# Kernel tuning notes

Hardware: AMD Instinct MI355X
Metric: run time of the kernel (lower is better)

## Reference

```python
import jax, jax.numpy as jnp
import numpy as np

N_NODES = 20000
N_EDGES = 1280000
IN_CH = 256
HID_CH = 256


def setup_inputs() -> dict:
    key = jax.random.key(0)
    ks = jax.random.split(key, 8)
    s = 1.0 / np.sqrt(IN_CH)
    sh = 1.0 / np.sqrt(HID_CH)
    return {
        "x": jax.random.normal(ks[0], (N_NODES, IN_CH), dtype=jnp.float32),
        "edge_index": jax.random.randint(ks[1], (2, N_EDGES), 0, N_NODES, dtype=jnp.int64),
        "W1_l": jax.random.normal(ks[2], (HID_CH, IN_CH), dtype=jnp.float32) * s,
        "b1": jnp.zeros((HID_CH,), dtype=jnp.float32),
        "W1_r": jax.random.normal(ks[3], (HID_CH, IN_CH), dtype=jnp.float32) * s,
        "W2_l": jax.random.normal(ks[4], (1, HID_CH), dtype=jnp.float32) * sh,
        "b2": jnp.zeros((1,), dtype=jnp.float32),
        "W2_r": jax.random.normal(ks[5], (1, HID_CH), dtype=jnp.float32) * sh,
        "fc_w": jax.random.normal(ks[6], (1, N_NODES), dtype=jnp.float32) * (1.0 / np.sqrt(N_NODES)),
        "fc_b": jnp.zeros((1,), dtype=jnp.float32),
    }


def _sage(x, src, dst, inv_deg, W_l, b, W_r):
    # mean-aggregate source features at destination nodes, then two linears
    agg = jax.ops.segment_sum(x[src], dst, num_segments=N_NODES)  # [N, C]
    mean = agg * inv_deg[:, None]
    return mean @ W_l.T + b + x @ W_r.T


def reference(x, edge_index, W1_l, b1, W1_r, W2_l, b2, W2_r, fc_w, fc_b):
    src, dst = edge_index[0], edge_index[1]
    deg = jax.ops.segment_sum(jnp.ones((dst.shape[0],), dtype=x.dtype), dst,
                              num_segments=N_NODES)
    inv_deg = 1.0 / jnp.maximum(deg, 1.0)  # isolated nodes -> 0 aggregate
    h = jax.nn.relu(_sage(x, src, dst, inv_deg, W1_l, b1, W1_r))   # [N, H]
    h = jax.nn.relu(_sage(h, src, dst, inv_deg, W2_l, b2, W2_r))   # [N, 1]
    h = h[:, 0]                                                     # squeeze dim 1
    return h @ fc_w[0] + fc_b                                       # [1]
```

## Files before the change

kernel.cpp:

```cpp
#include <hip/hip_runtime.h>

#define N_NODESC 20000
#define N_EDGESC 1280000
#define NB 256
#define EPB 5000

typedef short bf16x8 __attribute__((ext_vector_type(8)));
typedef float f32x4 __attribute__((ext_vector_type(4)));

constexpr size_t OFF_DEG      = 0;
constexpr size_t OFF_ROWSTART = 81920;
constexpr size_t OFF_INVDEG   = 163840;
constexpr size_t OFF_BSUM     = 245760;
constexpr size_t OFF_BOFF     = 246272;
constexpr size_t OFF_S1       = 246784;
constexpr size_t OFF_T1       = 326784;
constexpr size_t OFF_PART     = 406784;
constexpr size_t OFF_HIST     = 427264;
constexpr size_t OFF_CSR      = 10667264;
constexpr size_t OFF_XB       = 13227392;
constexpr size_t OFF_MEANB    = 23467392;
constexpr size_t OFF_W1LB     = 33707392;
constexpr size_t OFF_W1RB     = 33838464;

static __device__ __forceinline__ unsigned f2bf(float f) {
    unsigned u = __float_as_uint(f);
    return ((u + 0x7fffu + ((u >> 16) & 1u)) >> 16) & 0xffffu;
}
static __device__ __forceinline__ float bflo(unsigned w) {
    return __uint_as_float(w << 16);
}
static __device__ __forceinline__ float bfhi(unsigned w) {
    return __uint_as_float(w & 0xffff0000u);
}

__global__ void __launch_bounds__(256) k_cast(
        const float4* __restrict__ x, const float4* __restrict__ w1l,
        const float4* __restrict__ w1r, uint4* __restrict__ xb,
        uint4* __restrict__ w1lb, uint4* __restrict__ w1rb,
        float* __restrict__ s1, float* __restrict__ t1,
        int* __restrict__ bsum) {
    int g = blockIdx.x * 256 + threadIdx.x;
    if (g < N_NODESC) { s1[g] = 0.0f; t1[g] = 0.0f; }
    if (g < 128) bsum[g] = 0;
    const float4* src; uint4* dst; int off;
    if (g < 640000)      { src = x;   dst = xb;   off = g; }
    else if (g < 648192) { src = w1l; dst = w1lb; off = g - 640000; }
    else                 { src = w1r; dst = w1rb; off = g - 648192; }
    float4 a = src[off * 2], b = src[off * 2 + 1];
    uint4 o;
    o.x = f2bf(a.x) | (f2bf(a.y) << 16);
    o.y = f2bf(a.z) | (f2bf(a.w) << 16);
    o.z = f2bf(b.x) | (f2bf(b.y) << 16);
    o.w = f2bf(b.z) | (f2bf(b.w) << 16);
    dst[off] = o;
}

__global__ void __launch_bounds__(256) k_hist(const int* __restrict__ ei,
                                              unsigned short* __restrict__ hist) {
    __shared__ unsigned int lh[10000];
    int b = blockIdx.x, t = threadIdx.x;
    for (int w = t; w < 10000; w += 256) lh[w] = 0;
    __syncthreads();
    int base = b * EPB;
    for (int i = t; i < EPB; i += 256) {
        int d = ei[N_EDGESC + base + i];
        atomicAdd(&lh[d >> 1], (d & 1) ? 0x10000u : 1u);
    }
    __syncthreads();
    unsigned int* gh = (unsigned int*)(hist + (size_t)b * N_NODESC);
    for (int w = t; w < 10000; w += 256) gh[w] = lh[w];
}

__global__ void __launch_bounds__(256) k_prefix(unsigned short* __restrict__ hist,
                                                int* __restrict__ deg,
                                                int* __restrict__ bsum) {
    __shared__ int wtot[4][64];
    int t = threadIdx.x;
    int lb = t & 63, sub = t >> 6;
    int bin = blockIdx.x * 64 + lb;
    bool ok = bin < N_NODESC;
    int vals[64];
    int run = 0;
    if (ok) {
        #pragma unroll
        for (int i = 0; i < 64; i++) {
            vals[i] = hist[(size_t)(sub * 64 + i) * N_NODESC + bin];
            run += vals[i];
        }
    }
    wtot[sub][lb] = run;
    __syncthreads();
    int off = 0, total = 0;
    for (int w = 0; w < 4; w++) {
        int v = wtot[w][lb];
        if (w < sub) off += v;
        total += v;
    }
    if (sub == 0) {
        int tv = ok ? total : 0;
        if (ok) deg[bin] = total;
        #pragma unroll
        for (int o2 = 32; o2 > 0; o2 >>= 1) tv += __shfl_down(tv, o2);
        if (lb == 0) atomicAdd(&bsum[(blockIdx.x * 64) >> 8], tv);
    }
    if (ok) {
        int run2 = off;
        #pragma unroll
        for (int i = 0; i < 64; i++) {
            hist[(size_t)(sub * 64 + i) * N_NODESC + bin] = (unsigned short)run2;
            run2 += vals[i];
        }
    }
}

__global__ void k_scan2(const int* __restrict__ bsum, int* __restrict__ boff,
                        int* __restrict__ row_start) {
    __shared__ int sm[128];
    int t = threadIdx.x;
    int v = (t < 79) ? bsum[t] : 0;
    sm[t] = v;
    __syncthreads();
    for (int off = 1; off < 128; off <<= 1) {
        int add = (t >= off) ? sm[t - off] : 0;
        __syncthreads();
        sm[t] += add;
        __syncthreads();
    }
    if (t < 79) boff[t] = sm[t] - v;
    if (t == 0) row_start[N_NODESC] = sm[127];
}

__global__ void __launch_bounds__(256) k_scan3(
        const int* __restrict__ deg, const int* __restrict__ boff,
        int* __restrict__ row_start, float* __restrict__ inv_deg) {
    __shared__ int wsum[4];
    int i = blockIdx.x * 256 + threadIdx.x;
    int lane = threadIdx.x & 63, wid = threadIdx.x >> 6;
    int v = (i < N_NODESC) ? deg[i] : 0;
    int incl = v;
    #pragma unroll
    for (int off = 1; off < 64; off <<= 1) {
        int n = __shfl_up(incl, off);
        if (lane >= off) incl += n;
    }
    if (lane == 63) wsum[wid] = incl;
    __syncthreads();
    int wpre = 0;
    #pragma unroll
    for (int w = 0; w < 4; w++) wpre += (w < wid) ? wsum[w] : 0;
    if (i < N_NODESC) {
        row_start[i] = boff[blockIdx.x] + wpre + incl - v;
        inv_deg[i]   = 1.0f / (float)max(v, 1);
    }
}

__global__ void __launch_bounds__(256) k_fill2(const int* __restrict__ ei,
        const int* __restrict__ row_start, const unsigned short* __restrict__ hist,
        unsigned short* __restrict__ csr) {
    __shared__ unsigned int lh[10000];
    int b = blockIdx.x, t = threadIdx.x;
    for (int w = t; w < 10000; w += 256) lh[w] = 0;
    __syncthreads();
    int base = b * EPB;
    const unsigned short* hb = hist + (size_t)b * N_NODESC;
    for (int i = t; i < EPB; i += 256) {
        int e = base + i;
        int d = ei[N_EDGESC + e];
        int s = ei[e];
        unsigned int old = atomicAdd(&lh[d >> 1], (d & 1) ? 0x10000u : 1u);
        int rank = (d & 1) ? (int)(old >> 16) : (int)(old & 0xffffu);
        int pos = row_start[d] + (int)hb[d] + rank;
        csr[pos] = (unsigned short)s;
    }
}

__global__ void __launch_bounds__(256) k_agg(const char* __restrict__ xbc,
        const int* __restrict__ row_start, const unsigned short* __restrict__ csr,
        const float* __restrict__ inv_deg, uint4* __restrict__ meanb4) {
    int wid = threadIdx.x >> 6, lane = threadIdx.x & 63;
    int node = blockIdx.x * 4 + wid;
    int pass = blockIdx.y;
    int ol = lane & 7, oct = lane >> 3;
    unsigned lanebyte = ((unsigned)(pass << 3) + (unsigned)ol) << 4;
    int start = row_start[node], end = row_start[node + 1];
    float a0=0.f,a1=0.f,a2=0.f,a3=0.f,a4=0.f,a5=0.f,a6=0.f,a7=0.f;
    float c0=0.f,c1=0.f,c2=0.f,c3=0.f,c4=0.f,c5=0.f,c6=0.f,c7=0.f;
    int idx = (start < end) ? (int)csr[start + lane] : 0;
    for (int j = start; j < end; j += 64) {
        int cnt = min(64, end - j);
        int idxn = (j + 64 < end) ? (int)csr[j + 64 + lane] : 0;
        int fs = cnt >> 3;
        int k = 0;
        for (; k + 2 <= fs; k += 2) {
            int s0 = __shfl(idx, 8 * k + oct);
            int s1 = __shfl(idx, 8 * k + 8 + oct);
            uint4 v0 = *(const uint4*)(xbc + (((unsigned)s0 << 9) + lanebyte));
            uint4 v1 = *(const uint4*)(xbc + (((unsigned)s1 << 9) + lanebyte));
            a0 += bflo(v0.x); a1 += bfhi(v0.x); a2 += bflo(v0.y); a3 += bfhi(v0.y);
            a4 += bflo(v0.z); a5 += bfhi(v0.z); a6 += bflo(v0.w); a7 += bfhi(v0.w);
            c0 += bflo(v1.x); c1 += bfhi(v1.x); c2 += bflo(v1.y); c3 += bfhi(v1.y);
            c4 += bflo(v1.z); c5 += bfhi(v1.z); c6 += bflo(v1.w); c7 += bfhi(v1.w);
        }
        if (k < fs) {
            int s0 = __shfl(idx, 8 * k + oct);
            uint4 v = *(const uint4*)(xbc + (((unsigned)s0 << 9) + lanebyte));
            a0 += bflo(v.x); a1 += bfhi(v.x); a2 += bflo(v.y); a3 += bfhi(v.y);
            a4 += bflo(v.z); a5 += bfhi(v.z); a6 += bflo(v.w); a7 += bfhi(v.w);
        }
        int rem = cnt & 7;
        if (rem) {
            int s0 = __shfl(idx, 8 * fs + oct);
            if (oct < rem) {
                uint4 v = *(const uint4*)(xbc + (((unsigned)s0 << 9) + lanebyte));
                c0 += bflo(v.x); c1 += bfhi(v.x); c2 += bflo(v.y); c3 += bfhi(v.y);
                c4 += bflo(v.z); c5 += bfhi(v.z); c6 += bflo(v.w); c7 += bfhi(v.w);
            }
        }
        idx = idxn;
    }
    a0 += c0; a1 += c1; a2 += c2; a3 += c3;
    a4 += c4; a5 += c5; a6 += c6; a7 += c7;
    a0 += __shfl_down(a0, 32); a1 += __shfl_down(a1, 32);
    a2 += __shfl_down(a2, 32); a3 += __shfl_down(a3, 32);
    a4 += __shfl_down(a4, 32); a5 += __shfl_down(a5, 32);
    a6 += __shfl_down(a6, 32); a7 += __shfl_down(a7, 32);
    a0 += __shfl_down(a0, 16); a1 += __shfl_down(a1, 16);
    a2 += __shfl_down(a2, 16); a3 += __shfl_down(a3, 16);
    a4 += __shfl_down(a4, 16); a5 += __shfl_down(a5, 16);
    a6 += __shfl_down(a6, 16); a7 += __shfl_down(a7, 16);
    a0 += __shfl_down(a0, 8);  a1 += __shfl_down(a1, 8);
    a2 += __shfl_down(a2, 8);  a3 += __shfl_down(a3, 8);
    a4 += __shfl_down(a4, 8);  a5 += __shfl_down(a5, 8);
    a6 += __shfl_down(a6, 8);  a7 += __shfl_down(a7, 8);
    if (oct == 0) {
        float inv = inv_deg[node];
        uint4 o;
        o.x = f2bf(a0 * inv) | (f2bf(a1 * inv) << 16);
        o.y = f2bf(a2 * inv) | (f2bf(a3 * inv) << 16);
        o.z = f2bf(a4 * inv) | (f2bf(a5 * inv) << 16);
        o.w = f2bf(a6 * inv) | (f2bf(a7 * inv) << 16);
        meanb4[(size_t)node * 32 + (pass << 3) + ol] = o;
    }
}

__global__ void __launch_bounds__(256) k_gemm(const uint4* __restrict__ meanb4,
        const uint4* __restrict__ xb4, const uint4* __restrict__ w1lb4,
        const uint4* __restrict__ w1rb4, const float* __restrict__ b1,
        const float* __restrict__ w2l, const float* __restrict__ w2r,
        float* __restrict__ s1, float* __restrict__ t1) {
    __shared__ __align__(16) unsigned short As[64][72];
    __shared__ __align__(16) unsigned short Bs[64][72];
    int t = threadIdx.x;
    int m0 = blockIdx.x * 64, n0 = blockIdx.y * 64;
    int wv = t >> 6, l = t & 63, lr = l & 15, quad = l >> 4;
    f32x4 acc[4] = {{0,0,0,0},{0,0,0,0},{0,0,0,0},{0,0,0,0}};
    for (int kt = 0; kt < 8; kt++) {
        const uint4* Asrc = (kt < 4) ? meanb4 : xb4;
        const uint4* Bsrc = (kt < 4) ? w1lb4 : w1rb4;
        int k0q = (kt & 3) * 8;
        #pragma unroll
        for (int p = 0; p < 2; p++) {
            int f = t + p * 256;
            int row = f >> 3, cc = f & 7;
            int m = m0 + row;
            uint4 va = (m < N_NODESC) ? Asrc[(size_t)m * 32 + k0q + cc]
                                      : make_uint4(0, 0, 0, 0);
            uint4 vb = Bsrc[(size_t)(n0 + row) * 32 + k0q + cc];
            *(uint4*)&As[row][cc * 8] = va;
            *(uint4*)&Bs[row][cc * 8] = vb;
        }
        __syncthreads();
        #pragma unroll
        for (int ks = 0; ks < 64; ks += 32) {
            bf16x8 af = *(const bf16x8*)&As[wv * 16 + lr][ks + quad * 8];
            #pragma unroll
            for (int jj = 0; jj < 4; jj++) {
                bf16x8 bf = *(const bf16x8*)&Bs[jj * 16 + lr][ks + quad * 8];
                acc[jj] = __builtin_amdgcn_mfma_f32_16x16x32_bf16(
                              af, bf, acc[jj], 0, 0, 0);
            }
        }
        __syncthreads();
    }
    float ps[4] = {0, 0, 0, 0}, pt[4] = {0, 0, 0, 0};
    #pragma unroll
    for (int jj = 0; jj < 4; jj++) {
        int col = n0 + jj * 16 + lr;
        float bb = b1[col], wl = w2l[col], wr = w2r[col];
        #pragma unroll
        for (int r = 0; r < 4; r++) {
            float h = fmaxf(acc[jj][r] + bb, 0.0f);
            ps[r] += h * wl; pt[r] += h * wr;
        }
    }
    #pragma unroll
    for (int r = 0; r < 4; r++) {
        #pragma unroll
        for (int off = 8; off > 0; off >>= 1) {
            ps[r] += __shfl_down(ps[r], off, 16);
            pt[r] += __shfl_down(pt[r], off, 16);
        }
    }
    if (lr == 0) {
        int mb = m0 + wv * 16 + quad * 4;
        #pragma unroll
        for (int r = 0; r < 4; r++) {
            int m = mb + r;
            if (m < N_NODESC) {
                atomicAdd(&s1[m], ps[r]);
                atomicAdd(&t1[m], pt[r]);
            }
        }
    }
}

__global__ void __launch_bounds__(256) k_layer2(
        const int* __restrict__ row_start, const unsigned short* __restrict__ csr,
        const float* __restrict__ inv_deg, const float* __restrict__ s1,
        const float* __restrict__ t1, const float* __restrict__ b2,
        const float* __restrict__ fc_w, float* __restrict__ part) {
    __shared__ float pw[4];
    int wid = threadIdx.x >> 6, lane = threadIdx.x & 63;
    int node = blockIdx.x * 4 + wid;
    float contrib = 0.0f;
    if (node < N_NODESC) {
        int start = row_start[node], end = row_start[node + 1];
        float s = 0.0f;
        for (int j = start + lane; j < end; j += 64) s += s1[csr[j]];
        #pragma unroll
        for (int off = 32; off > 0; off >>= 1) s += __shfl_down(s, off);
        if (lane == 0) {
            float h2 = fmaxf(s * inv_deg[node] + b2[0] + t1[node], 0.0f);
            contrib = h2 * fc_w[node];
        }
    }
    if (lane == 0) pw[wid] = contrib;
    __syncthreads();
    if (threadIdx.x == 0)
        part[blockIdx.x] = pw[0] + pw[1] + pw[2] + pw[3];
}

__global__ void __launch_bounds__(256) k_final(const float* __restrict__ part,
        const float* __restrict__ fc_b, float* __restrict__ out) {
    __shared__ float sm[4];
    int t = threadIdx.x;
    float s = 0.0f;
    for (int i = t; i < 5000; i += 256) s += part[i];
    #pragma unroll
    for (int off = 32; off > 0; off >>= 1) s += __shfl_down(s, off);
    if ((t & 63) == 0) sm[t >> 6] = s;
    __syncthreads();
    if (t == 0) out[0] = sm[0] + sm[1] + sm[2] + sm[3] + fc_b[0];
}

extern "C" void kernel_launch(void* const* d_in, const int* in_sizes, int n_in,
                              void* d_out, int out_size, void* d_ws, size_t ws_size,
                              hipStream_t stream) {
    const float* x    = (const float*)d_in[0];
    const int*   ei   = (const int*)d_in[1];
    const float* w1l  = (const float*)d_in[2];
    const float* b1   = (const float*)d_in[3];
    const float* w1r  = (const float*)d_in[4];
    const float* w2l  = (const float*)d_in[5];
    const float* b2   = (const float*)d_in[6];
    const float* w2r  = (const float*)d_in[7];
    const float* fcw  = (const float*)d_in[8];
    const float* fcb  = (const float*)d_in[9];
    float* out = (float*)d_out;

    char* ws = (char*)d_ws;
    int*    deg       = (int*)(ws + OFF_DEG);
    int*    row_start = (int*)(ws + OFF_ROWSTART);
    float*  inv_deg   = (float*)(ws + OFF_INVDEG);
    int*    bsum      = (int*)(ws + OFF_BSUM);
    int*    boff      = (int*)(ws + OFF_BOFF);
    float*  s1        = (float*)(ws + OFF_S1);
    float*  t1        = (float*)(ws + OFF_T1);
    float*  part      = (float*)(ws + OFF_PART);
    unsigned short* hist = (unsigned short*)(ws + OFF_HIST);
    unsigned short* csr  = (unsigned short*)(ws + OFF_CSR);
    char*   xbc       = (char*)(ws + OFF_XB);
    uint4*  meanb4    = (uint4*)(ws + OFF_MEANB);
    uint4*  w1lb4     = (uint4*)(ws + OFF_W1LB);
    uint4*  w1rb4     = (uint4*)(ws + OFF_W1RB);

    k_cast<<<2564, 256, 0, stream>>>((const float4*)x, (const float4*)w1l,
                                     (const float4*)w1r, (uint4*)xbc,
                                     w1lb4, w1rb4, s1, t1, bsum);
    k_hist<<<NB, 256, 0, stream>>>(ei, hist);
    k_prefix<<<313, 256, 0, stream>>>(hist, deg, bsum);
    k_scan2<<<1, 128, 0, stream>>>(bsum, boff, row_start);
    k_scan3<<<79, 256, 0, stream>>>(deg, boff, row_start, inv_deg);
    k_fill2<<<NB, 256, 0, stream>>>(ei, row_start, hist, csr);
    dim3 agrid(5000, 4);
    k_agg<<<agrid, 256, 0, stream>>>(xbc, row_start, csr, inv_deg, meanb4);
    dim3 ggrid(313, 4);
    k_gemm<<<ggrid, 256, 0, stream>>>(meanb4, (const uint4*)xbc,
                                      w1lb4, w1rb4, b1, w2l, w2r, s1, t1);
    k_layer2<<<5000, 256, 0, stream>>>(row_start, csr, inv_deg, s1, t1, b2,
                                       fcw, part);
    k_final<<<1, 256, 0, stream>>>(part, fcb, out);
}
```

Measured before the change: 216.4 us.

## Build CSR with global atomic degree counts and cursors instead of per-block histograms

Replaces the per-block shared-memory histogram, column prefix over 256 block histograms, and rank-based fill with a global atomic degree count, a small block-sum reduction, and an atomic cursor fill. This removes the large histogram write and read traffic and two heavy kernels. In exchange it relies on global atomics (1.28M per pass, twice) and makes the order of neighbours within each CSR row nondeterministic, which can change float summation order in aggregation.

```diff
diff --git a/kernel.cpp b/kernel.cpp
--- a/kernel.cpp
+++ b/kernel.cpp
@@ -2,8 +2,6 @@
 
 #define N_NODESC 20000
 #define N_EDGESC 1280000
-#define NB 256
-#define EPB 5000
 
 typedef short bf16x8 __attribute__((ext_vector_type(8)));
 typedef float f32x4 __attribute__((ext_vector_type(4)));
@@ -16,7 +14,7 @@
 constexpr size_t OFF_S1       = 246784;
 constexpr size_t OFF_T1       = 326784;
 constexpr size_t OFF_PART     = 406784;
-constexpr size_t OFF_HIST     = 427264;
+constexpr size_t OFF_CURSOR   = 427264;
 constexpr size_t OFF_CSR      = 10667264;
 constexpr size_t OFF_XB       = 13227392;
 constexpr size_t OFF_MEANB    = 23467392;
@@ -39,10 +37,9 @@
         const float4* __restrict__ w1r, uint4* __restrict__ xb,
         uint4* __restrict__ w1lb, uint4* __restrict__ w1rb,
         float* __restrict__ s1, float* __restrict__ t1,
-        int* __restrict__ bsum) {
+        int* __restrict__ deg) {
     int g = blockIdx.x * 256 + threadIdx.x;
-    if (g < N_NODESC) { s1[g] = 0.0f; t1[g] = 0.0f; }
-    if (g < 128) bsum[g] = 0;
+    if (g < N_NODESC) { s1[g] = 0.0f; t1[g] = 0.0f; deg[g] = 0; }
     const float4* src; uint4* dst; int off;
     if (g < 640000)      { src = x;   dst = xb;   off = g; }
     else if (g < 648192) { src = w1l; dst = w1lb; off = g - 640000; }
@@ -56,62 +53,28 @@
     dst[off] = o;
 }
 
-__global__ void __launch_bounds__(256) k_hist(const int* __restrict__ ei,
-                                              unsigned short* __restrict__ hist) {
-    __shared__ unsigned int lh[10000];
-    int b = blockIdx.x, t = threadIdx.x;
-    for (int w = t; w < 10000; w += 256) lh[w] = 0;
-    __syncthreads();
-    int base = b * EPB;
-    for (int i = t; i < EPB; i += 256) {
-        int d = ei[N_EDGESC + base + i];
-        atomicAdd(&lh[d >> 1], (d & 1) ? 0x10000u : 1u);
-    }
-    __syncthreads();
-    unsigned int* gh = (unsigned int*)(hist + (size_t)b * N_NODESC);
-    for (int w = t; w < 10000; w += 256) gh[w] = lh[w];
-}
-
-__global__ void __launch_bounds__(256) k_prefix(unsigned short* __restrict__ hist,
-                                                int* __restrict__ deg,
-                                                int* __restrict__ bsum) {
-    __shared__ int wtot[4][64];
-    int t = threadIdx.x;
-    int lb = t & 63, sub = t >> 6;
-    int bin = blockIdx.x * 64 + lb;
-    bool ok = bin < N_NODESC;
-    int vals[64];
-    int run = 0;
-    if (ok) {
-        #pragma unroll
-        for (int i = 0; i < 64; i++) {
-            vals[i] = hist[(size_t)(sub * 64 + i) * N_NODESC + bin];
-            run += vals[i];
-        }
-    }
-    wtot[sub][lb] = run;
-    __syncthreads();
-    int off = 0, total = 0;
-    for (int w = 0; w < 4; w++) {
-        int v = wtot[w][lb];
-        if (w < sub) off += v;
-        total += v;
-    }
-    if (sub == 0) {
-        int tv = ok ? total : 0;
-        if (ok) deg[bin] = total;
-        #pragma unroll
-        for (int o2 = 32; o2 > 0; o2 >>= 1) tv += __shfl_down(tv, o2);
-        if (lb == 0) atomicAdd(&bsum[(blockIdx.x * 64) >> 8], tv);
-    }
-    if (ok) {
-        int run2 = off;
-        #pragma unroll
-        for (int i = 0; i < 64; i++) {
-            hist[(size_t)(sub * 64 + i) * N_NODESC + bin] = (unsigned short)run2;
-            run2 += vals[i];
-        }
-    }
+__global__ void __launch_bounds__(256) k_deg(const int4* __restrict__ dst4,
+                                             int* __restrict__ deg) {
+    int i = blockIdx.x * 256 + threadIdx.x;
+    int4 d = dst4[i];
+    atomicAdd(&deg[d.x], 1);
+    atomicAdd(&deg[d.y], 1);
+    atomicAdd(&deg[d.z], 1);
+    atomicAdd(&deg[d.w], 1);
+}
+
+__global__ void __launch_bounds__(256) k_bsum(const int* __restrict__ deg,
+                                              int* __restrict__ bsum) {
+    __shared__ int sm[4];
+    int i = blockIdx.x * 256 + threadIdx.x;
+    int lane = threadIdx.x & 63, wid = threadIdx.x >> 6;
+    int v = (i < N_NODESC) ? deg[i] : 0;
+    #pragma unroll
+    for (int off = 32; off > 0; off >>= 1) v += __shfl_down(v, off);
+    if (lane == 0) sm[wid] = v;
+    __syncthreads();
+    if (threadIdx.x == 0)
+        bsum[blockIdx.x] = sm[0] + sm[1] + sm[2] + sm[3];
 }
 
 __global__ void k_scan2(const int* __restrict__ bsum, int* __restrict__ boff,
@@ -133,7 +96,8 @@
 
 __global__ void __launch_bounds__(256) k_scan3(
         const int* __restrict__ deg, const int* __restrict__ boff,
-        int* __restrict__ row_start, float* __restrict__ inv_deg) {
+        int* __restrict__ row_start, float* __restrict__ inv_deg,
+        int* __restrict__ cursor) {
     __shared__ int wsum[4];
     int i = blockIdx.x * 256 + threadIdx.x;
     int lane = threadIdx.x & 63, wid = threadIdx.x >> 6;
@@ -150,29 +114,27 @@
     #pragma unroll
     for (int w = 0; w < 4; w++) wpre += (w < wid) ? wsum[w] : 0;
     if (i < N_NODESC) {
-        row_start[i] = boff[blockIdx.x] + wpre + incl - v;
+        int rs = boff[blockIdx.x] + wpre + incl - v;
+        row_start[i] = rs;
+        cursor[i]    = rs;
         inv_deg[i]   = 1.0f / (float)max(v, 1);
     }
 }
 
-__global__ void __launch_bounds__(256) k_fill2(const int* __restrict__ ei,
-        const int* __restrict__ row_start, const unsigned short* __restrict__ hist,
+__global__ void __launch_bounds__(256) k_fill(const int4* __restrict__ src4,
+        const int4* __restrict__ dst4, int* __restrict__ cursor,
         unsigned short* __restrict__ csr) {
-    __shared__ unsigned int lh[10000];
-    int b = blockIdx.x, t = threadIdx.x;
-    for (int w = t; w < 10000; w += 256) lh[w] = 0;
-    __syncthreads();
-    int base = b * EPB;
-    const unsigned short* hb = hist + (size_t)b * N_NODESC;
-    for (int i = t; i < EPB; i += 256) {
-        int e = base + i;
-        int d = ei[N_EDGESC + e];
-        int s = ei[e];
-        unsigned int old = atomicAdd(&lh[d >> 1], (d & 1) ? 0x10000u : 1u);
-        int rank = (d & 1) ? (int)(old >> 16) : (int)(old & 0xffffu);
-        int pos = row_start[d] + (int)hb[d] + rank;
-        csr[pos] = (unsigned short)s;
-    }
+    int i = blockIdx.x * 256 + threadIdx.x;
+    int4 s = src4[i];
+    int4 d = dst4[i];
+    int p0 = atomicAdd(&cursor[d.x], 1);
+    int p1 = atomicAdd(&cursor[d.y], 1);
+    int p2 = atomicAdd(&cursor[d.z], 1);
+    int p3 = atomicAdd(&cursor[d.w], 1);
+    csr[p0] = (unsigned short)s.x;
+    csr[p1] = (unsigned short)s.y;
+    csr[p2] = (unsigned short)s.z;
+    csr[p3] = (unsigned short)s.w;
 }
 
 __global__ void __launch_bounds__(256) k_agg(const char* __restrict__ xbc,
@@ -378,21 +340,24 @@
     float*  s1        = (float*)(ws + OFF_S1);
     float*  t1        = (float*)(ws + OFF_T1);
     float*  part      = (float*)(ws + OFF_PART);
-    unsigned short* hist = (unsigned short*)(ws + OFF_HIST);
+    int*    cursor    = (int*)(ws + OFF_CURSOR);
     unsigned short* csr  = (unsigned short*)(ws + OFF_CSR);
     char*   xbc       = (char*)(ws + OFF_XB);
     uint4*  meanb4    = (uint4*)(ws + OFF_MEANB);
     uint4*  w1lb4     = (uint4*)(ws + OFF_W1LB);
     uint4*  w1rb4     = (uint4*)(ws + OFF_W1RB);
 
+    const int4* src4 = (const int4*)ei;
+    const int4* dst4 = (const int4*)(ei + N_EDGESC);
+
     k_cast<<<2564, 256, 0, stream>>>((const float4*)x, (const float4*)w1l,
                                      (const float4*)w1r, (uint4*)xbc,
-                                     w1lb4, w1rb4, s1, t1, bsum);
-    k_hist<<<NB, 256, 0, stream>>>(ei, hist);
-    k_prefix<<<313, 256, 0, stream>>>(hist, deg, bsum);
+                                     w1lb4, w1rb4, s1, t1, deg);
+    k_deg<<<1250, 256, 0, stream>>>(dst4, deg);
+    k_bsum<<<79, 256, 0, stream>>>(deg, bsum);
     k_scan2<<<1, 128, 0, stream>>>(bsum, boff, row_start);
-    k_scan3<<<79, 256, 0, stream>>>(deg, boff, row_start, inv_deg);
-    k_fill2<<<NB, 256, 0, stream>>>(ei, row_start, hist, csr);
+    k_scan3<<<79, 256, 0, stream>>>(deg, boff, row_start, inv_deg, cursor);
+    k_fill<<<1250, 256, 0, stream>>>(src4, dst4, cursor, csr);
     dim3 agrid(5000, 4);
     k_agg<<<agrid, 256, 0, stream>>>(xbc, row_start, csr, inv_deg, meanb4);
     dim3 ggrid(313, 4);
```

Measured after the change: 302.7 us. 39.9% more time.
